# Kernel optimization log

Measured on AMD Instinct MI355X. Metric: run time of the kernel, lower is better.

The kernel has to match this reference:

```python
import jax, jax.numpy as jnp
import numpy as np

B, IN, H, OUT, E = 4096, 1024, 2048, 1024, 16

def setup_inputs() -> dict:
    key = jax.random.key(0)
    ks = jax.random.split(key, 8)
    def lin_init(k, shape, fan_in):
        bound = 1.0 / np.sqrt(fan_in)
        return jax.random.uniform(k, shape, jnp.float32, -bound, bound)
    return {
        "obs": jax.random.normal(ks[0], (B, IN), jnp.float32),
        "switch_idx": jax.random.randint(ks[1], (B,), 0, E, jnp.int32),
        "pre_w": lin_init(ks[2], (H, IN), IN),
        "pre_b": lin_init(ks[3], (H,), IN),
        "expert_w": lin_init(ks[4], (E, H, H), H),
        "expert_b": lin_init(ks[5], (E, H), H),
        "post_w": lin_init(ks[6], (OUT, H), H),
        "post_b": lin_init(ks[7], (OUT,), H),
    }

def reference(obs, switch_idx, pre_w, pre_b, expert_w, expert_b, post_w, post_b):
    # pre_switch: Linear + Tanh
    x = jnp.tanh(obs @ pre_w.T + pre_b)                      # [B, H]
    # compute ALL switch experts (faithful to torch.stack over switches)
    all_x = jnp.einsum("bi,eoi->beo", x, expert_w) + expert_b  # [B, E, H]
    # gather the selected expert output per sample
    x = jnp.take_along_axis(all_x, switch_idx[:, None, None].astype(jnp.int32), axis=1)[:, 0]  # [B, H]
    # post_switch: Tanh, Linear, Tanh
    x = jnp.tanh(x)
    return jnp.tanh(x @ post_w.T + post_b)                   # [B, OUT]
```

## Files before the change

kernel.cpp:

```cpp
#include <hip/hip_runtime.h>


#define Bsz 4096
#define INd 1024
#define Hd  2048
#define OUTd 1024
#define NEXP 16

#define BM 128
#define BN 128
#define BK 32
#define LDT 56

typedef short bf16x8 __attribute__((ext_vector_type(8)));
typedef float f32x4 __attribute__((ext_vector_type(4)));
typedef unsigned short u16;

__device__ __forceinline__ u16 f2bf(float f) {
  unsigned u = __float_as_uint(f);
  u += 0x7FFF + ((u >> 16) & 1);
  return (u16)(u >> 16);
}

__device__ __forceinline__ float fast_tanh(float x) {
  float ax = fabsf(x);
  float e = __expf(2.0f * ax);
  float t = 1.0f - 2.0f / (e + 1.0f);
  return x < 0.0f ? -t : t;
}

__device__ __forceinline__ void mfma_step(const u16* As, const u16* Bs,
                                          int wm, int wn, int fr, int fk,
                                          f32x4 acc[4][4]) {
  bf16x8 af[4], bq[4];
#pragma unroll
  for (int i = 0; i < 4; ++i) af[i] = *(const bf16x8*)&As[(wm + 16 * i + fr) * LDT + fk];
#pragma unroll
  for (int j = 0; j < 4; ++j) bq[j] = *(const bf16x8*)&Bs[(wn + 16 * j + fr) * LDT + fk];
#pragma unroll
  for (int i = 0; i < 4; ++i)
#pragma unroll
    for (int j = 0; j < 4; ++j)
      acc[i][j] = __builtin_amdgcn_mfma_f32_16x16x32_bf16(af[i], bq[j], acc[i][j], 0, 0, 0);
}

__global__ __launch_bounds__(256) void k_bucket(const int* __restrict__ idx,
                                                int* __restrict__ offs,
                                                int* __restrict__ rows) {
  __shared__ int cnt[NEXP];
  __shared__ int base[NEXP];
  int t = threadIdx.x;
  if (t < NEXP) cnt[t] = 0;
  __syncthreads();
  for (int b = t; b < Bsz; b += 256) atomicAdd(&cnt[idx[b]], 1);
  __syncthreads();
  if (t == 0) {
    int s = 0;
    for (int e = 0; e < NEXP; ++e) { base[e] = s; offs[e] = s; s += cnt[e]; }
    offs[NEXP] = s;
  }
  __syncthreads();
  for (int b = t; b < Bsz; b += 256) {
    int e = idx[b];
    int p = atomicAdd(&base[e], 1);
    rows[p] = b;
  }
}

__global__ __launch_bounds__(256) void k_pre(const float* __restrict__ obs,
                                             const float* __restrict__ pre_w,
                                             const float* __restrict__ pre_b,
                                             u16* __restrict__ X1) {
  __shared__ u16 As[BM * LDT];
  __shared__ u16 Bs[BN * LDT];
  const int n0 = blockIdx.x * BN;
  const int m0 = blockIdx.y * BM;
  const int tid = threadIdx.x;
  const int lane = tid & 63;
  const int wv = tid >> 6;
  const int wm = (wv >> 1) * 64, wn = (wv & 1) * 64;
  const int fr = lane & 15, fq = lane >> 4;
  const int fk = fq * 8;
  const int sr = tid >> 3;
  const int skc = (tid & 7) * 4;

  f32x4 acc[4][4] = {};

  for (int k0 = 0; k0 < INd; k0 += BK) {
#pragma unroll
    for (int p = 0; p < 4; ++p) {
      int row = sr + 32 * p;
      float4 va = *(const float4*)&obs[(size_t)(m0 + row) * INd + k0 + skc];
      ushort4 ha; ha.x = f2bf(va.x); ha.y = f2bf(va.y); ha.z = f2bf(va.z); ha.w = f2bf(va.w);
      *(ushort4*)&As[row * LDT + skc] = ha;
      float4 vb = *(const float4*)&pre_w[(size_t)(n0 + row) * INd + k0 + skc];
      ushort4 hb; hb.x = f2bf(vb.x); hb.y = f2bf(vb.y); hb.z = f2bf(vb.z); hb.w = f2bf(vb.w);
      *(ushort4*)&Bs[row * LDT + skc] = hb;
    }
    __syncthreads();
    mfma_step(As, Bs, wm, wn, fr, fk, acc);
    __syncthreads();
  }
#pragma unroll
  for (int j = 0; j < 4; ++j) {
    int col = n0 + wn + 16 * j + fr;
    float bias = pre_b[col];
#pragma unroll
    for (int i = 0; i < 4; ++i) {
      int rb = m0 + wm + 16 * i + fq * 4;
#pragma unroll
      for (int r = 0; r < 4; ++r)
        X1[(size_t)(rb + r) * Hd + col] = f2bf(fast_tanh(acc[i][j][r] + bias));
    }
  }
}

__global__ __launch_bounds__(256) void k_expert(const u16* __restrict__ X1,
                                                const float* __restrict__ ew,
                                                const float* __restrict__ eb,
                                                const int* __restrict__ offs,
                                                const int* __restrict__ rows,
                                                u16* __restrict__ Z) {
  __shared__ u16 As[BM * LDT];
  __shared__ u16 Bs[BN * LDT];
  const int e = blockIdx.y >> 5;
  const int rt = blockIdx.y & 31;
  const int seg = offs[e];
  const int cnt = offs[e + 1] - seg;
  const int tbase = rt * BM;
  if (tbase >= cnt) return;
  const int nval = min(BM, cnt - tbase);
  const int n0 = blockIdx.x * BN;
  const float* We = ew + (size_t)e * Hd * Hd;

  const int tid = threadIdx.x;
  const int lane = tid & 63;
  const int wv = tid >> 6;
  const int wm = (wv >> 1) * 64, wn = (wv & 1) * 64;
  const int fr = lane & 15, fq = lane >> 4;
  const int fk = fq * 8;

  const int ar_ = tid >> 2;
  const int akc = (tid & 3) * 8;
  int rowg[2];
#pragma unroll
  for (int p = 0; p < 2; ++p) {
    int ar = ar_ + 64 * p;
    rowg[p] = (ar < nval) ? rows[seg + tbase + ar] : -1;
  }
  const int sr = tid >> 3;
  const int skc = (tid & 7) * 4;

  f32x4 acc[4][4] = {};
  const float4 zero4 = {0.f, 0.f, 0.f, 0.f};

  for (int k0 = 0; k0 < Hd; k0 += BK) {
#pragma unroll
    for (int p = 0; p < 2; ++p) {
      int ar = ar_ + 64 * p;
      float4 v = (rowg[p] >= 0) ? *(const float4*)&X1[(size_t)rowg[p] * Hd + k0 + akc] : zero4;
      *(float4*)&As[ar * LDT + akc] = v;
    }
#pragma unroll
    for (int p = 0; p < 4; ++p) {
      int row = sr + 32 * p;
      float4 vb = *(const float4*)&We[(size_t)(n0 + row) * Hd + k0 + skc];
      ushort4 hb; hb.x = f2bf(vb.x); hb.y = f2bf(vb.y); hb.z = f2bf(vb.z); hb.w = f2bf(vb.w);
      *(ushort4*)&Bs[row * LDT + skc] = hb;
    }
    __syncthreads();
    mfma_step(As, Bs, wm, wn, fr, fk, acc);
    __syncthreads();
  }
#pragma unroll
  for (int i = 0; i < 4; ++i) {
#pragma unroll
    for (int r = 0; r < 4; ++r) {
      int arow = wm + 16 * i + fq * 4 + r;
      if (arow < nval) {
        int orow = rows[seg + tbase + arow];
#pragma unroll
        for (int j = 0; j < 4; ++j) {
          int col = n0 + wn + 16 * j + fr;
          float bias = eb[(size_t)e * Hd + col];
          Z[(size_t)orow * Hd + col] = f2bf(fast_tanh(acc[i][j][r] + bias));
        }
      }
    }
  }
}

__global__ __launch_bounds__(256) void k_post(const u16* __restrict__ Z,
                                              const float* __restrict__ pw,
                                              const float* __restrict__ pb,
                                              float* __restrict__ out) {
  __shared__ u16 As[BM * LDT];
  __shared__ u16 Bs[BN * LDT];
  const int n0 = blockIdx.x * BN;
  const int m0 = blockIdx.y * BM;
  const int tid = threadIdx.x;
  const int lane = tid & 63;
  const int wv = tid >> 6;
  const int wm = (wv >> 1) * 64, wn = (wv & 1) * 64;
  const int fr = lane & 15, fq = lane >> 4;
  const int fk = fq * 8;
  const int ar_ = tid >> 2;
  const int akc = (tid & 3) * 8;
  const int sr = tid >> 3;
  const int skc = (tid & 7) * 4;

  f32x4 acc[4][4] = {};

  for (int k0 = 0; k0 < Hd; k0 += BK) {
#pragma unroll
    for (int p = 0; p < 2; ++p) {
      int ar = ar_ + 64 * p;
      float4 v = *(const float4*)&Z[(size_t)(m0 + ar) * Hd + k0 + akc];
      *(float4*)&As[ar * LDT + akc] = v;
    }
#pragma unroll
    for (int p = 0; p < 4; ++p) {
      int row = sr + 32 * p;
      float4 vb = *(const float4*)&pw[(size_t)(n0 + row) * Hd + k0 + skc];
      ushort4 hb; hb.x = f2bf(vb.x); hb.y = f2bf(vb.y); hb.z = f2bf(vb.z); hb.w = f2bf(vb.w);
      *(ushort4*)&Bs[row * LDT + skc] = hb;
    }
    __syncthreads();
    mfma_step(As, Bs, wm, wn, fr, fk, acc);
    __syncthreads();
  }
#pragma unroll
  for (int j = 0; j < 4; ++j) {
    int col = n0 + wn + 16 * j + fr;
    float bias = pb[col];
#pragma unroll
    for (int i = 0; i < 4; ++i) {
      int rb = m0 + wm + 16 * i + fq * 4;
#pragma unroll
      for (int r = 0; r < 4; ++r)
        out[(size_t)(rb + r) * OUTd + col] = fast_tanh(acc[i][j][r] + bias);
    }
  }
}

extern "C" void kernel_launch(void* const* d_in, const int* in_sizes, int n_in,
                              void* d_out, int out_size, void* d_ws, size_t ws_size,
                              hipStream_t stream) {
  const float* obs   = (const float*)d_in[0];
  const int*   sw    = (const int*)d_in[1];
  const float* pre_w = (const float*)d_in[2];
  const float* pre_b = (const float*)d_in[3];
  const float* ew    = (const float*)d_in[4];
  const float* eb    = (const float*)d_in[5];
  const float* pw    = (const float*)d_in[6];
  const float* pb    = (const float*)d_in[7];
  float* out = (float*)d_out;

  char* ws = (char*)d_ws;
  u16* X1   = (u16*)ws;
  u16* Z    = (u16*)(ws + (size_t)Bsz * Hd * 2);
  int* offs = (int*)(ws + (size_t)2 * Bsz * Hd * 2);
  int* rows = offs + 32;

  k_bucket<<<dim3(1), dim3(256), 0, stream>>>(sw, offs, rows);
  k_pre<<<dim3(Hd / BN, Bsz / BM), dim3(256), 0, stream>>>(obs, pre_w, pre_b, X1);
  k_expert<<<dim3(Hd / BN, NEXP * 32), dim3(256), 0, stream>>>(X1, ew, eb, offs, rows, Z);
  k_post<<<dim3(OUTd / BN, Bsz / BM), dim3(256), 0, stream>>>(Z, pw, pb, out);
}
```

Baseline: 649.6 us.

## Stage bf16 tiles via direct global-to-LDS loads with XOR-swizzled unpadded layout

Replaces the padded LDS tiles with unpadded 32-wide tiles that use an XOR swizzle to avoid bank conflicts. The bf16 activation tiles (gathered X1 rows in the expert GEMM, Z in the post GEMM) are now loaded with global_load_lds 16-byte transfers, so they no longer pass through registers. Gathered rows with no data point at a zeroed scratch buffer. The post GEMM moves to 64-row tiles to launch more blocks, and fp32 weight staging now uses 8-element vector loads. These changes add dependence on the swizzle being consistent between the writers and readers, and on a zero buffer being initialised by the bucket kernel.

```diff
diff --git a/kernel.cpp b/kernel.cpp
--- a/kernel.cpp
+++ b/kernel.cpp
@@ -7,11 +7,6 @@
 #define OUTd 1024
 #define NEXP 16
 
-#define BM 128
-#define BN 128
-#define BK 32
-#define LDT 56
-
 typedef short bf16x8 __attribute__((ext_vector_type(8)));
 typedef float f32x4 __attribute__((ext_vector_type(4)));
 typedef unsigned short u16;
@@ -29,16 +24,66 @@
   return x < 0.0f ? -t : t;
 }
 
-__device__ __forceinline__ void mfma_step(const u16* As, const u16* Bs,
-                                          int wm, int wn, int fr, int fk,
-                                          f32x4 acc[4][4]) {
-  bf16x8 af[4], bq[4];
-#pragma unroll
-  for (int i = 0; i < 4; ++i) af[i] = *(const bf16x8*)&As[(wm + 16 * i + fr) * LDT + fk];
-#pragma unroll
-  for (int j = 0; j < 4; ++j) bq[j] = *(const bf16x8*)&Bs[(wn + 16 * j + fr) * LDT + fk];
-#pragma unroll
-  for (int i = 0; i < 4; ++i)
+#define GLL16(g, l)                                                            \
+  __builtin_amdgcn_global_load_lds(                                            \
+      (const __attribute__((address_space(1))) unsigned int*)(g),              \
+      (__attribute__((address_space(3))) unsigned int*)(l), 16, 0, 0)
+
+__device__ __forceinline__ int swz(int r) { return (r ^ (r >> 2)) & 3; }
+
+__device__ __forceinline__ void stage_bf16_128(const u16* g, int ldk, u16* lds, int t) {
+  const int r0 = t >> 2;
+  const int c = (t & 3) ^ swz(r0);
+#pragma unroll
+  for (int p = 0; p < 2; ++p)
+    GLL16(g + (size_t)(r0 + 64 * p) * ldk + c * 8, lds + ((t + 256 * p) << 3));
+}
+
+__device__ __forceinline__ void stage_bf16_64(const u16* g, int ldk, u16* lds, int t) {
+  const int r = t >> 2;
+  const int c = (t & 3) ^ swz(r);
+  GLL16(g + (size_t)r * ldk + c * 8, lds + (t << 3));
+}
+
+__device__ __forceinline__ void stage_gather(const u16* X1k, const int rg[2],
+                                             const u16* zeroc, u16* lds, int t) {
+  const int r0 = t >> 2;
+  const int c = (t & 3) ^ swz(r0);
+#pragma unroll
+  for (int p = 0; p < 2; ++p) {
+    const u16* g = (rg[p] >= 0) ? X1k + (size_t)rg[p] * Hd + c * 8 : zeroc;
+    GLL16(g, lds + ((t + 256 * p) << 3));
+  }
+}
+
+__device__ __forceinline__ void stage_f32_128(const float* g, int ldk, u16* lds, int t) {
+  const int r0 = t >> 2;
+  const int c = (t & 3) ^ swz(r0);
+#pragma unroll
+  for (int p = 0; p < 2; ++p) {
+    const float* src = g + (size_t)(r0 + 64 * p) * ldk + c * 8;
+    float4 a = *(const float4*)src;
+    float4 b = *(const float4*)(src + 4);
+    bf16x8 o;
+    o[0] = (short)f2bf(a.x); o[1] = (short)f2bf(a.y);
+    o[2] = (short)f2bf(a.z); o[3] = (short)f2bf(a.w);
+    o[4] = (short)f2bf(b.x); o[5] = (short)f2bf(b.y);
+    o[6] = (short)f2bf(b.z); o[7] = (short)f2bf(b.w);
+    *(bf16x8*)&lds[(t + 256 * p) << 3] = o;
+  }
+}
+
+template <int MI>
+__device__ __forceinline__ void compute_tile(const u16* As, const u16* Bs,
+                                             int wm, int wn, int fr, int co,
+                                             f32x4 (&acc)[MI][4]) {
+  bf16x8 af[MI], bq[4];
+#pragma unroll
+  for (int i = 0; i < MI; ++i) af[i] = *(const bf16x8*)&As[(wm + 16 * i + fr) * 32 + co];
+#pragma unroll
+  for (int j = 0; j < 4; ++j) bq[j] = *(const bf16x8*)&Bs[(wn + 16 * j + fr) * 32 + co];
+#pragma unroll
+  for (int i = 0; i < MI; ++i)
 #pragma unroll
     for (int j = 0; j < 4; ++j)
       acc[i][j] = __builtin_amdgcn_mfma_f32_16x16x32_bf16(af[i], bq[j], acc[i][j], 0, 0, 0);
@@ -46,10 +91,12 @@
 
 __global__ __launch_bounds__(256) void k_bucket(const int* __restrict__ idx,
                                                 int* __restrict__ offs,
-                                                int* __restrict__ rows) {
+                                                int* __restrict__ rows,
+                                                int* __restrict__ zc) {
   __shared__ int cnt[NEXP];
   __shared__ int base[NEXP];
   int t = threadIdx.x;
+  if (t < 16) zc[t] = 0;
   if (t < NEXP) cnt[t] = 0;
   __syncthreads();
   for (int b = t; b < Bsz; b += 256) atomicAdd(&cnt[idx[b]], 1);
@@ -71,46 +118,35 @@
                                              const float* __restrict__ pre_w,
                                              const float* __restrict__ pre_b,
                                              u16* __restrict__ X1) {
-  __shared__ u16 As[BM * LDT];
-  __shared__ u16 Bs[BN * LDT];
-  const int n0 = blockIdx.x * BN;
-  const int m0 = blockIdx.y * BM;
-  const int tid = threadIdx.x;
-  const int lane = tid & 63;
-  const int wv = tid >> 6;
-  const int wm = (wv >> 1) * 64, wn = (wv & 1) * 64;
+  __shared__ u16 As[128 * 32];
+  __shared__ u16 Bs[128 * 32];
+  const int tid = threadIdx.x, lane = tid & 63, wv = tid >> 6;
+  const int wm = (wv >> 1) << 6, wn = (wv & 1) << 6;
   const int fr = lane & 15, fq = lane >> 4;
-  const int fk = fq * 8;
-  const int sr = tid >> 3;
-  const int skc = (tid & 7) * 4;
-
+  const int co = (fq ^ swz(fr)) << 3;
+  const int n0 = blockIdx.x * 128, m0 = blockIdx.y * 128;
   f32x4 acc[4][4] = {};
 
-  for (int k0 = 0; k0 < INd; k0 += BK) {
-#pragma unroll
-    for (int p = 0; p < 4; ++p) {
-      int row = sr + 32 * p;
-      float4 va = *(const float4*)&obs[(size_t)(m0 + row) * INd + k0 + skc];
-      ushort4 ha; ha.x = f2bf(va.x); ha.y = f2bf(va.y); ha.z = f2bf(va.z); ha.w = f2bf(va.w);
-      *(ushort4*)&As[row * LDT + skc] = ha;
-      float4 vb = *(const float4*)&pre_w[(size_t)(n0 + row) * INd + k0 + skc];
-      ushort4 hb; hb.x = f2bf(vb.x); hb.y = f2bf(vb.y); hb.z = f2bf(vb.z); hb.w = f2bf(vb.w);
-      *(ushort4*)&Bs[row * LDT + skc] = hb;
-    }
-    __syncthreads();
-    mfma_step(As, Bs, wm, wn, fr, fk, acc);
-    __syncthreads();
-  }
+  const float* Ab = obs + (size_t)m0 * INd;
+  const float* Bb = pre_w + (size_t)n0 * INd;
+  for (int k0 = 0; k0 < INd; k0 += 32) {
+    stage_f32_128(Ab + k0, INd, As, tid);
+    stage_f32_128(Bb + k0, INd, Bs, tid);
+    __syncthreads();
+    compute_tile<4>(As, Bs, wm, wn, fr, co, acc);
+    __syncthreads();
+  }
+
 #pragma unroll
   for (int j = 0; j < 4; ++j) {
     int col = n0 + wn + 16 * j + fr;
     float bias = pre_b[col];
 #pragma unroll
     for (int i = 0; i < 4; ++i) {
-      int rb = m0 + wm + 16 * i + fq * 4;
+      int rb2 = m0 + wm + 16 * i + fq * 4;
 #pragma unroll
       for (int r = 0; r < 4; ++r)
-        X1[(size_t)(rb + r) * Hd + col] = f2bf(fast_tanh(acc[i][j][r] + bias));
+        X1[(size_t)(rb2 + r) * Hd + col] = f2bf(fast_tanh(acc[i][j][r] + bias));
     }
   }
 }
@@ -120,58 +156,43 @@
                                                 const float* __restrict__ eb,
                                                 const int* __restrict__ offs,
                                                 const int* __restrict__ rows,
+                                                const u16* __restrict__ zeroc,
                                                 u16* __restrict__ Z) {
-  __shared__ u16 As[BM * LDT];
-  __shared__ u16 Bs[BN * LDT];
-  const int e = blockIdx.y >> 5;
-  const int rt = blockIdx.y & 31;
-  const int seg = offs[e];
-  const int cnt = offs[e + 1] - seg;
-  const int tbase = rt * BM;
+  const int e = blockIdx.y >> 5, rt = blockIdx.y & 31;
+  const int seg = offs[e], cnt = offs[e + 1] - seg;
+  const int tbase = rt * 128;
   if (tbase >= cnt) return;
-  const int nval = min(BM, cnt - tbase);
-  const int n0 = blockIdx.x * BN;
-  const float* We = ew + (size_t)e * Hd * Hd;
-
-  const int tid = threadIdx.x;
-  const int lane = tid & 63;
-  const int wv = tid >> 6;
-  const int wm = (wv >> 1) * 64, wn = (wv & 1) * 64;
+  const int nval = min(128, cnt - tbase);
+  const int n0 = blockIdx.x * 128;
+
+  __shared__ u16 As[128 * 32];
+  __shared__ u16 Bs[128 * 32];
+  const int tid = threadIdx.x, lane = tid & 63, wv = tid >> 6;
+  const int wm = (wv >> 1) << 6, wn = (wv & 1) << 6;
   const int fr = lane & 15, fq = lane >> 4;
-  const int fk = fq * 8;
-
-  const int ar_ = tid >> 2;
-  const int akc = (tid & 3) * 8;
-  int rowg[2];
-#pragma unroll
-  for (int p = 0; p < 2; ++p) {
-    int ar = ar_ + 64 * p;
-    rowg[p] = (ar < nval) ? rows[seg + tbase + ar] : -1;
-  }
-  const int sr = tid >> 3;
-  const int skc = (tid & 7) * 4;
-
+  const int co = (fq ^ swz(fr)) << 3;
+
+  int rg[2];
+  {
+    const int r0 = tid >> 2;
+#pragma unroll
+    for (int p = 0; p < 2; ++p) {
+      int ar = r0 + 64 * p;
+      rg[p] = (ar < nval) ? rows[seg + tbase + ar] : -1;
+    }
+  }
+
+  const float* We = ew + (size_t)e * Hd * Hd + (size_t)n0 * Hd;
   f32x4 acc[4][4] = {};
-  const float4 zero4 = {0.f, 0.f, 0.f, 0.f};
-
-  for (int k0 = 0; k0 < Hd; k0 += BK) {
-#pragma unroll
-    for (int p = 0; p < 2; ++p) {
-      int ar = ar_ + 64 * p;
-      float4 v = (rowg[p] >= 0) ? *(const float4*)&X1[(size_t)rowg[p] * Hd + k0 + akc] : zero4;
-      *(float4*)&As[ar * LDT + akc] = v;
-    }
-#pragma unroll
-    for (int p = 0; p < 4; ++p) {
-      int row = sr + 32 * p;
-      float4 vb = *(const float4*)&We[(size_t)(n0 + row) * Hd + k0 + skc];
-      ushort4 hb; hb.x = f2bf(vb.x); hb.y = f2bf(vb.y); hb.z = f2bf(vb.z); hb.w = f2bf(vb.w);
-      *(ushort4*)&Bs[row * LDT + skc] = hb;
-    }
-    __syncthreads();
-    mfma_step(As, Bs, wm, wn, fr, fk, acc);
-    __syncthreads();
-  }
+
+  for (int k0 = 0; k0 < Hd; k0 += 32) {
+    stage_gather(X1 + k0, rg, zeroc, As, tid);
+    stage_f32_128(We + k0, Hd, Bs, tid);
+    __syncthreads();
+    compute_tile<4>(As, Bs, wm, wn, fr, co, acc);
+    __syncthreads();
+  }
+
 #pragma unroll
   for (int i = 0; i < 4; ++i) {
 #pragma unroll
@@ -194,51 +215,35 @@
                                               const float* __restrict__ pw,
                                               const float* __restrict__ pb,
                                               float* __restrict__ out) {
-  __shared__ u16 As[BM * LDT];
-  __shared__ u16 Bs[BN * LDT];
-  const int n0 = blockIdx.x * BN;
-  const int m0 = blockIdx.y * BM;
-  const int tid = threadIdx.x;
-  const int lane = tid & 63;
-  const int wv = tid >> 6;
-  const int wm = (wv >> 1) * 64, wn = (wv & 1) * 64;
+  __shared__ u16 As[64 * 32];
+  __shared__ u16 Bs[128 * 32];
+  const int tid = threadIdx.x, lane = tid & 63, wv = tid >> 6;
+  const int wm = (wv >> 1) << 5, wn = (wv & 1) << 6;
   const int fr = lane & 15, fq = lane >> 4;
-  const int fk = fq * 8;
-  const int ar_ = tid >> 2;
-  const int akc = (tid & 3) * 8;
-  const int sr = tid >> 3;
-  const int skc = (tid & 7) * 4;
-
-  f32x4 acc[4][4] = {};
-
-  for (int k0 = 0; k0 < Hd; k0 += BK) {
-#pragma unroll
-    for (int p = 0; p < 2; ++p) {
-      int ar = ar_ + 64 * p;
-      float4 v = *(const float4*)&Z[(size_t)(m0 + ar) * Hd + k0 + akc];
-      *(float4*)&As[ar * LDT + akc] = v;
-    }
-#pragma unroll
-    for (int p = 0; p < 4; ++p) {
-      int row = sr + 32 * p;
-      float4 vb = *(const float4*)&pw[(size_t)(n0 + row) * Hd + k0 + skc];
-      ushort4 hb; hb.x = f2bf(vb.x); hb.y = f2bf(vb.y); hb.z = f2bf(vb.z); hb.w = f2bf(vb.w);
-      *(ushort4*)&Bs[row * LDT + skc] = hb;
-    }
-    __syncthreads();
-    mfma_step(As, Bs, wm, wn, fr, fk, acc);
-    __syncthreads();
-  }
+  const int co = (fq ^ swz(fr)) << 3;
+  const int n0 = blockIdx.x * 128, m0 = blockIdx.y * 64;
+  f32x4 acc[2][4] = {};
+
+  const u16* Ab = Z + (size_t)m0 * Hd;
+  const float* Bb = pw + (size_t)n0 * Hd;
+  for (int k0 = 0; k0 < Hd; k0 += 32) {
+    stage_bf16_64(Ab + k0, Hd, As, tid);
+    stage_f32_128(Bb + k0, Hd, Bs, tid);
+    __syncthreads();
+    compute_tile<2>(As, Bs, wm, wn, fr, co, acc);
+    __syncthreads();
+  }
+
 #pragma unroll
   for (int j = 0; j < 4; ++j) {
     int col = n0 + wn + 16 * j + fr;
     float bias = pb[col];
 #pragma unroll
-    for (int i = 0; i < 4; ++i) {
-      int rb = m0 + wm + 16 * i + fq * 4;
+    for (int i = 0; i < 2; ++i) {
+      int rb2 = m0 + wm + 16 * i + fq * 4;
 #pragma unroll
       for (int r = 0; r < 4; ++r)
-        out[(size_t)(rb + r) * OUTd + col] = fast_tanh(acc[i][j][r] + bias);
+        out[(size_t)(rb2 + r) * OUTd + col] = fast_tanh(acc[i][j][r] + bias);
     }
   }
 }
@@ -257,13 +262,15 @@
   float* out = (float*)d_out;
 
   char* ws = (char*)d_ws;
-  u16* X1   = (u16*)ws;
-  u16* Z    = (u16*)(ws + (size_t)Bsz * Hd * 2);
-  int* offs = (int*)(ws + (size_t)2 * Bsz * Hd * 2);
-  int* rows = offs + 32;
-
-  k_bucket<<<dim3(1), dim3(256), 0, stream>>>(sw, offs, rows);
-  k_pre<<<dim3(Hd / BN, Bsz / BM), dim3(256), 0, stream>>>(obs, pre_w, pre_b, X1);
-  k_expert<<<dim3(Hd / BN, NEXP * 32), dim3(256), 0, stream>>>(X1, ew, eb, offs, rows, Z);
-  k_post<<<dim3(OUTd / BN, Bsz / BM), dim3(256), 0, stream>>>(Z, pw, pb, out);
-}
+  int* offs  = (int*)ws;
+  int* rows  = (int*)(ws + 128);
+  u16* zeroc = (u16*)(ws + 128 + 16384);
+  const size_t MISC = 65536;
+  u16* X1 = (u16*)(ws + MISC);
+  u16* Zb = (u16*)(ws + MISC + ((size_t)Bsz * Hd * 2));
+
+  k_bucket<<<dim3(1), dim3(256), 0, stream>>>(sw, offs, rows, (int*)zeroc);
+  k_pre<<<dim3(Hd / 128, Bsz / 128), dim3(256), 0, stream>>>(obs, pre_w, pre_b, X1);
+  k_expert<<<dim3(Hd / 128, NEXP * 32), dim3(256), 0, stream>>>(X1, ew, eb, offs, rows, zeroc, Zb);
+  k_post<<<dim3(OUTd / 128, Bsz / 64), dim3(256), 0, stream>>>(Zb, pw, pb, out);
+}
```

New measurement: 632.9 us. 1.03x faster.
